# Kernel optimization log

Hardware: AMD Instinct MI355X
Metric: run time of the kernel (lower is better)

The kernel has to match this reference:

```python
import jax, jax.numpy as jnp
import numpy as np


def setup_inputs() -> dict:
    key = jax.random.key(0)
    k1, k2, k3 = jax.random.split(key, 3)
    B, C, H, W, D = 2, 32, 64, 64, 96
    NUM_CLASSES = 2
    features = jax.random.normal(k1, (B, C, H, W, D), dtype=jnp.float32)
    predictions = jax.random.normal(k2, (B, NUM_CLASSES, H, W, D), dtype=jnp.float32)
    targets = jax.random.randint(k3, (B, 1, H, W, D), 0, NUM_CLASSES, dtype=jnp.int64)
    return {"features": features, "predictions": predictions, "targets": targets}


def reference(features, predictions, targets):
    # features: (B,C,H,W,D), predictions: (B,K,H,W,D) logits, targets: (B,1,H,W,D) int
    B, C, H, W, D = features.shape
    K = predictions.shape[1]
    N = H * W * D

    probs = jax.nn.softmax(predictions, axis=1)          # (B,K,H,W,D)
    feat = features.reshape(B, C, N).transpose(0, 2, 1)  # (B,N,C)
    tgt = targets.reshape(B, N)                           # (B,N)
    probs = probs.reshape(B, K, N)                        # (B,K,N)

    onehot = jax.nn.one_hot(tgt, K, dtype=feat.dtype)     # (B,N,K)
    n_pix = onehot.sum(axis=1)                            # (B,K) pixel counts per class
    safe_n = jnp.maximum(n_pix, 1.0)

    # per-class spectral centers: masked mean over pixels
    centers = jnp.einsum('bnk,bnc->bkc', onehot, feat) / safe_n[..., None]  # (B,K,C)

    # gather each pixel's own-class center and confidence
    center_pp = jnp.einsum('bnk,bkc->bnc', onehot, centers)                 # (B,N,C)
    conf = jnp.take_along_axis(probs, tgt[:, None, :], axis=1)[:, 0, :]     # (B,N)

    dist = jnp.linalg.norm(feat - center_pp, axis=-1)     # (B,N) L2 spectral distance
    weighted = dist * conf

    # per-(b,class) mean of weighted distances over that class's pixels
    class_loss = jnp.einsum('bnk,bn->bk', onehot, weighted) / safe_n        # (B,K)

    valid = (n_pix >= 2.0).astype(feat.dtype)             # classes with >=2 pixels
    num_valid = valid.sum()
    total = (class_loss * valid).sum()
    return jnp.where(num_valid > 0, total / jnp.maximum(num_valid, 1.0),
                     jnp.zeros((), dtype=feat.dtype))
```

## Files before the change

### kernel.cpp

```cpp
#include <hip/hip_runtime.h>
#include <math.h>

#define CCH 32
#define KCLS 2
#define BB 2
#define SSEG 32
#define P1_BLOCKS (BB * SSEG * CCH)
#define P2_PER_B 768
#define P2_BLOCKS (BB * P2_PER_B)

#define OFF_PART 0
#define OFF_CNTP (OFF_PART + P1_BLOCKS * 2)
#define OFF_CTR  (OFF_CNTP + BB * SSEG)
#define OFF_CNT  (OFF_CTR + BB * KCLS * CCH)
#define OFF_LOSS (OFF_CNT + BB * KCLS)

__device__ __forceinline__ float waveReduceSum(float v) {
#pragma unroll
    for (int o = 32; o > 0; o >>= 1) v += __shfl_down(v, o);
    return v;
}

__global__ void __launch_bounds__(256) scl_pass1(
    const float* __restrict__ feat, const int* __restrict__ tgt,
    float* __restrict__ part, float* __restrict__ cntPart, int N) {
    const int blk = blockIdx.x;
    const int c = blk & (CCH - 1);
    const int s = (blk >> 5) & (SSEG - 1);
    const int b = blk >> 10;
    const int segVox = N / SSEG;
    const int segQ = segVox / 4;

    const float* fb = feat + ((size_t)(b * CCH + c)) * N + (size_t)s * segVox;
    const int*   tb = tgt + (size_t)b * N + (size_t)s * segVox;

    float s1 = 0.f, st = 0.f, c1 = 0.f;
    for (int q = threadIdx.x; q < segQ; q += 256) {
        const int n = q * 4;
        const int4   t4 = *reinterpret_cast<const int4*>(tb + n);
        const float4 v  = *reinterpret_cast<const float4*>(fb + n);
        const float m1x = t4.x ? 1.f : 0.f;
        const float m1y = t4.y ? 1.f : 0.f;
        const float m1z = t4.z ? 1.f : 0.f;
        const float m1w = t4.w ? 1.f : 0.f;
        st += (v.x + v.y) + (v.z + v.w);
        s1 += v.x * m1x + v.y * m1y + v.z * m1z + v.w * m1w;
        c1 += (m1x + m1y) + (m1z + m1w);
    }

    __shared__ float sm[4][3];
    const int lane = threadIdx.x & 63;
    const int wv   = threadIdx.x >> 6;
    float r1 = waveReduceSum(s1);
    float rt = waveReduceSum(st);
    float rc = waveReduceSum(c1);
    if (lane == 0) { sm[wv][0] = r1; sm[wv][1] = rt; sm[wv][2] = rc; }
    __syncthreads();
    if (threadIdx.x == 0) {
        const float a1 = sm[0][0] + sm[1][0] + sm[2][0] + sm[3][0];
        const float at = sm[0][1] + sm[1][1] + sm[2][1] + sm[3][1];
        part[blk * 2 + 0] = a1;
        part[blk * 2 + 1] = at;
        if (c == 0) {
            const float ac = sm[0][2] + sm[1][2] + sm[2][2] + sm[3][2];
            cntPart[b * SSEG + s] = ac;
        }
    }
}

__global__ void scl_reduce(const float* __restrict__ part,
                           const float* __restrict__ cntPart,
                           float* __restrict__ centers,
                           float* __restrict__ counts, int N) {
    __shared__ float cs[BB * 2];
    const int t = threadIdx.x;
    if (t < BB) {
        float c1 = 0.f;
#pragma unroll
        for (int s = 0; s < SSEG; ++s) c1 += cntPart[t * SSEG + s];
        const float c0 = (float)N - c1;
        cs[t * 2 + 0] = c0; cs[t * 2 + 1] = c1;
        counts[t * 2 + 0] = c0; counts[t * 2 + 1] = c1;
    }
    __syncthreads();
    if (t < BB * CCH) {
        const int b = t >> 5, c = t & 31;
        float s1 = 0.f, stt = 0.f;
#pragma unroll
        for (int s = 0; s < SSEG; ++s) {
            const float* p = part + ((size_t)((b * SSEG + s) * CCH + c)) * 2;
            s1  += p[0];
            stt += p[1];
        }
        const float c0 = cs[b * 2 + 0], c1v = cs[b * 2 + 1];
        centers[(b * KCLS + 0) * CCH + c] = (stt - s1) / fmaxf(c0, 1.f);
        centers[(b * KCLS + 1) * CCH + c] = s1 / fmaxf(c1v, 1.f);
    }
}

__global__ void __launch_bounds__(256) scl_pass2(
    const float* __restrict__ feat, const float* __restrict__ pred,
    const int* __restrict__ tgt, const float* __restrict__ centers,
    float* __restrict__ lossPart, int N) {
    const int blk = blockIdx.x;
    const int b  = (blk >= P2_PER_B) ? 1 : 0;
    const int lb = blk - b * P2_PER_B;

    __shared__ float ctr[KCLS * CCH];
    if (threadIdx.x < KCLS * CCH)
        ctr[threadIdx.x] = centers[b * KCLS * CCH + threadIdx.x];
    __syncthreads();

    const int n = (lb * 256 + threadIdx.x) * 2;
    const float* fb = feat + (size_t)b * CCH * N;
    const float* p0 = pred + (size_t)b * KCLS * N;
    const float* p1 = p0 + N;
    const int*   tb = tgt + (size_t)b * N;

    const int2   t2 = *reinterpret_cast<const int2*>(tb + n);
    const float2 a0 = *reinterpret_cast<const float2*>(p0 + n);
    const float2 a1 = *reinterpret_cast<const float2*>(p1 + n);

    float d2x = 0.f, d2y = 0.f;
#pragma unroll
    for (int c = 0; c < CCH; ++c) {
        const float2 v = *reinterpret_cast<const float2*>(fb + (size_t)c * N + n);
        const float c0 = ctr[c], c1 = ctr[CCH + c];
        float d;
        d = v.x - (t2.x ? c1 : c0); d2x += d * d;
        d = v.y - (t2.y ? c1 : c0); d2y += d * d;
    }

    float l0 = 0.f, l1 = 0.f;
    {
        float mx = fmaxf(a0.x, a1.x);
        float e0 = __expf(a0.x - mx), e1 = __expf(a1.x - mx);
        float cf = (t2.x ? e1 : e0) / (e0 + e1);
        float w  = sqrtf(d2x) * cf;
        l0 += t2.x ? 0.f : w; l1 += t2.x ? w : 0.f;
        mx = fmaxf(a0.y, a1.y);
        e0 = __expf(a0.y - mx); e1 = __expf(a1.y - mx);
        cf = (t2.y ? e1 : e0) / (e0 + e1);
        w  = sqrtf(d2y) * cf;
        l0 += t2.y ? 0.f : w; l1 += t2.y ? w : 0.f;
    }

    __shared__ float sm[4][2];
    const int lane = threadIdx.x & 63;
    const int wv   = threadIdx.x >> 6;
    float r0 = waveReduceSum(l0);
    float r1 = waveReduceSum(l1);
    if (lane == 0) { sm[wv][0] = r0; sm[wv][1] = r1; }
    __syncthreads();
    if (threadIdx.x == 0) {
        lossPart[blk * 2 + 0] = sm[0][0] + sm[1][0] + sm[2][0] + sm[3][0];
        lossPart[blk * 2 + 1] = sm[0][1] + sm[1][1] + sm[2][1] + sm[3][1];
    }
}

__global__ void __launch_bounds__(256) scl_pass3(
    const float* __restrict__ lossPart, const float* __restrict__ counts,
    float* __restrict__ out) {
    float a00 = 0.f, a01 = 0.f, a10 = 0.f, a11 = 0.f;
    for (int blk = threadIdx.x; blk < P2_BLOCKS; blk += 256) {
        const float l0 = lossPart[blk * 2 + 0];
        const float l1 = lossPart[blk * 2 + 1];
        if (blk < P2_PER_B) { a00 += l0; a01 += l1; }
        else                { a10 += l0; a11 += l1; }
    }
    __shared__ float sm[4][4];
    const int lane = threadIdx.x & 63;
    const int wv   = threadIdx.x >> 6;
    float r0 = waveReduceSum(a00);
    float r1 = waveReduceSum(a01);
    float r2 = waveReduceSum(a10);
    float r3 = waveReduceSum(a11);
    if (lane == 0) { sm[wv][0] = r0; sm[wv][1] = r1; sm[wv][2] = r2; sm[wv][3] = r3; }
    __syncthreads();
    if (threadIdx.x == 0) {
        float loss[4];
#pragma unroll
        for (int i = 0; i < 4; ++i)
            loss[i] = sm[0][i] + sm[1][i] + sm[2][i] + sm[3][i];
        float total = 0.f, nv = 0.f;
#pragma unroll
        for (int bk = 0; bk < 4; ++bk) {
            const float cn = counts[bk];
            const float cl = loss[bk] / fmaxf(cn, 1.f);
            if (cn >= 2.f) { total += cl; nv += 1.f; }
        }
        out[0] = (nv > 0.f) ? (total / nv) : 0.f;
    }
}

extern "C" void kernel_launch(void* const* d_in, const int* in_sizes, int n_in,
                              void* d_out, int out_size, void* d_ws, size_t ws_size,
                              hipStream_t stream) {
    const float* feat = (const float*)d_in[0];
    const float* pred = (const float*)d_in[1];
    const int*   tgt  = (const int*)d_in[2];
    float* out = (float*)d_out;

    const int totalVox = in_sizes[2];
    const int N = totalVox / BB;

    float* ws       = (float*)d_ws;
    float* part     = ws + OFF_PART;
    float* cntPart  = ws + OFF_CNTP;
    float* centers  = ws + OFF_CTR;
    float* counts   = ws + OFF_CNT;
    float* lossPart = ws + OFF_LOSS;

    scl_pass1<<<P1_BLOCKS, 256, 0, stream>>>(feat, tgt, part, cntPart, N);
    scl_reduce<<<1, 64, 0, stream>>>(part, cntPart, centers, counts, N);
    scl_pass2<<<P2_BLOCKS, 256, 0, stream>>>(feat, pred, tgt, centers, lossPart, N);
    scl_pass3<<<1, 256, 0, stream>>>(lossPart, counts, out);
}
```

Before: 47.96 us.

## Fold center reduction into pass2 and finalize via last-block ticket

Removes the single-block center-reduction kernel and the final reduction kernel, cutting four launches to two. Each pass2 block now recomputes the per-batch centers from the pass1 partials in shared memory. A global atomic ticket, reset in pass1, lets the last pass2 block do the final loss reduction. This trades two launch gaps and their serialization for redundant small reductions in every pass2 block plus an atomic and threadfence per block.

```diff
diff --git a/kernel.cpp b/kernel.cpp
--- a/kernel.cpp
+++ b/kernel.cpp
@@ -11,9 +11,8 @@
 
 #define OFF_PART 0
 #define OFF_CNTP (OFF_PART + P1_BLOCKS * 2)
-#define OFF_CTR  (OFF_CNTP + BB * SSEG)
-#define OFF_CNT  (OFF_CTR + BB * KCLS * CCH)
-#define OFF_LOSS (OFF_CNT + BB * KCLS)
+#define OFF_LOSS (OFF_CNTP + BB * SSEG)
+#define OFF_TICK (OFF_LOSS + P2_BLOCKS * 2)
 
 __device__ __forceinline__ float waveReduceSum(float v) {
 #pragma unroll
@@ -23,7 +22,10 @@
 
 __global__ void __launch_bounds__(256) scl_pass1(
     const float* __restrict__ feat, const int* __restrict__ tgt,
-    float* __restrict__ part, float* __restrict__ cntPart, int N) {
+    float* __restrict__ part, float* __restrict__ cntPart,
+    unsigned int* __restrict__ ticket, int N) {
+    if (blockIdx.x == 0 && threadIdx.x == 0) *ticket = 0u;
+
     const int blk = blockIdx.x;
     const int c = blk & (CCH - 1);
     const int s = (blk >> 5) & (SSEG - 1);
@@ -57,61 +59,59 @@
     if (lane == 0) { sm[wv][0] = r1; sm[wv][1] = rt; sm[wv][2] = rc; }
     __syncthreads();
     if (threadIdx.x == 0) {
-        const float a1 = sm[0][0] + sm[1][0] + sm[2][0] + sm[3][0];
-        const float at = sm[0][1] + sm[1][1] + sm[2][1] + sm[3][1];
-        part[blk * 2 + 0] = a1;
-        part[blk * 2 + 1] = at;
-        if (c == 0) {
-            const float ac = sm[0][2] + sm[1][2] + sm[2][2] + sm[3][2];
-            cntPart[b * SSEG + s] = ac;
-        }
-    }
-}
-
-__global__ void scl_reduce(const float* __restrict__ part,
-                           const float* __restrict__ cntPart,
-                           float* __restrict__ centers,
-                           float* __restrict__ counts, int N) {
-    __shared__ float cs[BB * 2];
-    const int t = threadIdx.x;
-    if (t < BB) {
-        float c1 = 0.f;
-#pragma unroll
-        for (int s = 0; s < SSEG; ++s) c1 += cntPart[t * SSEG + s];
-        const float c0 = (float)N - c1;
-        cs[t * 2 + 0] = c0; cs[t * 2 + 1] = c1;
-        counts[t * 2 + 0] = c0; counts[t * 2 + 1] = c1;
-    }
-    __syncthreads();
-    if (t < BB * CCH) {
-        const int b = t >> 5, c = t & 31;
-        float s1 = 0.f, stt = 0.f;
-#pragma unroll
-        for (int s = 0; s < SSEG; ++s) {
-            const float* p = part + ((size_t)((b * SSEG + s) * CCH + c)) * 2;
-            s1  += p[0];
-            stt += p[1];
-        }
-        const float c0 = cs[b * 2 + 0], c1v = cs[b * 2 + 1];
-        centers[(b * KCLS + 0) * CCH + c] = (stt - s1) / fmaxf(c0, 1.f);
-        centers[(b * KCLS + 1) * CCH + c] = s1 / fmaxf(c1v, 1.f);
+        part[blk * 2 + 0] = sm[0][0] + sm[1][0] + sm[2][0] + sm[3][0];
+        part[blk * 2 + 1] = sm[0][1] + sm[1][1] + sm[2][1] + sm[3][1];
+        if (c == 0)
+            cntPart[b * SSEG + s] = sm[0][2] + sm[1][2] + sm[2][2] + sm[3][2];
     }
 }
 
 __global__ void __launch_bounds__(256) scl_pass2(
     const float* __restrict__ feat, const float* __restrict__ pred,
-    const int* __restrict__ tgt, const float* __restrict__ centers,
-    float* __restrict__ lossPart, int N) {
+    const int* __restrict__ tgt,
+    const float* __restrict__ part, const float* __restrict__ cntPart,
+    float* __restrict__ lossPart, unsigned int* __restrict__ ticket,
+    float* __restrict__ out, int N) {
     const int blk = blockIdx.x;
     const int b  = (blk >= P2_PER_B) ? 1 : 0;
     const int lb = blk - b * P2_PER_B;
-
+    const int t = threadIdx.x;
+
+    __shared__ float red[64][4];
+    __shared__ float cnt_sm[34];
     __shared__ float ctr[KCLS * CCH];
-    if (threadIdx.x < KCLS * CCH)
-        ctr[threadIdx.x] = centers[b * KCLS * CCH + threadIdx.x];
-    __syncthreads();
-
-    const int n = (lb * 256 + threadIdx.x) * 2;
+    if (t < SSEG) cnt_sm[t] = cntPart[b * SSEG + t];
+    {
+        const int combo = t >> 2;
+        const int quarter = t & 3;
+        const int c = combo >> 1;
+        const int val = combo & 1;
+        const float* p = part + ((size_t)(b * SSEG) * CCH + c) * 2 + val;
+        float s = 0.f;
+#pragma unroll
+        for (int i = 0; i < 8; ++i)
+            s += p[(size_t)(quarter * 8 + i) * CCH * 2];
+        red[combo][quarter] = s;
+    }
+    __syncthreads();
+    if (t == 0) {
+        float c1 = 0.f;
+#pragma unroll
+        for (int i = 0; i < SSEG; ++i) c1 += cnt_sm[i];
+        cnt_sm[32] = c1;
+    }
+    __syncthreads();
+    if (t < CCH) {
+        const float c1 = cnt_sm[32];
+        const float c0 = (float)N - c1;
+        const float s1 = (red[t*2][0] + red[t*2][1]) + (red[t*2][2] + red[t*2][3]);
+        const float st = (red[t*2+1][0] + red[t*2+1][1]) + (red[t*2+1][2] + red[t*2+1][3]);
+        ctr[t]       = (st - s1) / fmaxf(c0, 1.f);
+        ctr[CCH + t] = s1 / fmaxf(c1, 1.f);
+    }
+    __syncthreads();
+
+    const int n = (lb * 256 + t) * 2;
     const float* fb = feat + (size_t)b * CCH * N;
     const float* p0 = pred + (size_t)b * KCLS * N;
     const float* p1 = p0 + N;
@@ -145,49 +145,60 @@
         l0 += t2.y ? 0.f : w; l1 += t2.y ? w : 0.f;
     }
 
-    __shared__ float sm[4][2];
-    const int lane = threadIdx.x & 63;
-    const int wv   = threadIdx.x >> 6;
+    const int lane = t & 63;
+    const int wv   = t >> 6;
     float r0 = waveReduceSum(l0);
     float r1 = waveReduceSum(l1);
-    if (lane == 0) { sm[wv][0] = r0; sm[wv][1] = r1; }
-    __syncthreads();
-    if (threadIdx.x == 0) {
-        lossPart[blk * 2 + 0] = sm[0][0] + sm[1][0] + sm[2][0] + sm[3][0];
-        lossPart[blk * 2 + 1] = sm[0][1] + sm[1][1] + sm[2][1] + sm[3][1];
-    }
-}
-
-__global__ void __launch_bounds__(256) scl_pass3(
-    const float* __restrict__ lossPart, const float* __restrict__ counts,
-    float* __restrict__ out) {
+    __syncthreads();
+    if (lane == 0) { red[wv][0] = r0; red[wv][1] = r1; }
+    __syncthreads();
+
+    __shared__ bool isLast;
+    if (t == 0) {
+        lossPart[blk * 2 + 0] = (red[0][0] + red[1][0]) + (red[2][0] + red[3][0]);
+        lossPart[blk * 2 + 1] = (red[0][1] + red[1][1]) + (red[2][1] + red[3][1]);
+        __threadfence();
+        isLast = (atomicAdd(ticket, 1u) == P2_BLOCKS - 1);
+    }
+    __syncthreads();
+    if (!isLast) return;
+
+    __threadfence();
     float a00 = 0.f, a01 = 0.f, a10 = 0.f, a11 = 0.f;
-    for (int blk = threadIdx.x; blk < P2_BLOCKS; blk += 256) {
-        const float l0 = lossPart[blk * 2 + 0];
-        const float l1 = lossPart[blk * 2 + 1];
-        if (blk < P2_PER_B) { a00 += l0; a01 += l1; }
-        else                { a10 += l0; a11 += l1; }
-    }
-    __shared__ float sm[4][4];
-    const int lane = threadIdx.x & 63;
-    const int wv   = threadIdx.x >> 6;
-    float r0 = waveReduceSum(a00);
-    float r1 = waveReduceSum(a01);
-    float r2 = waveReduceSum(a10);
-    float r3 = waveReduceSum(a11);
-    if (lane == 0) { sm[wv][0] = r0; sm[wv][1] = r1; sm[wv][2] = r2; sm[wv][3] = r3; }
-    __syncthreads();
-    if (threadIdx.x == 0) {
+    for (int i = t; i < P2_BLOCKS; i += 256) {
+        const float l0e = lossPart[i * 2 + 0];
+        const float l1e = lossPart[i * 2 + 1];
+        if (i < P2_PER_B) { a00 += l0e; a01 += l1e; }
+        else              { a10 += l0e; a11 += l1e; }
+    }
+    float q0 = waveReduceSum(a00);
+    float q1 = waveReduceSum(a01);
+    float q2 = waveReduceSum(a10);
+    float q3 = waveReduceSum(a11);
+    __syncthreads();
+    if (lane == 0) { red[wv][0] = q0; red[wv][1] = q1; red[wv][2] = q2; red[wv][3] = q3; }
+    __syncthreads();
+    if (t == 0) {
         float loss[4];
 #pragma unroll
         for (int i = 0; i < 4; ++i)
-            loss[i] = sm[0][i] + sm[1][i] + sm[2][i] + sm[3][i];
+            loss[i] = (red[0][i] + red[1][i]) + (red[2][i] + red[3][i]);
+        float cn[4];
+        {
+            float c1b0 = 0.f, c1b1 = 0.f;
+#pragma unroll
+            for (int i = 0; i < SSEG; ++i) {
+                c1b0 += cntPart[i];
+                c1b1 += cntPart[SSEG + i];
+            }
+            cn[0] = (float)N - c1b0; cn[1] = c1b0;
+            cn[2] = (float)N - c1b1; cn[3] = c1b1;
+        }
         float total = 0.f, nv = 0.f;
 #pragma unroll
         for (int bk = 0; bk < 4; ++bk) {
-            const float cn = counts[bk];
-            const float cl = loss[bk] / fmaxf(cn, 1.f);
-            if (cn >= 2.f) { total += cl; nv += 1.f; }
+            const float cl = loss[bk] / fmaxf(cn[bk], 1.f);
+            if (cn[bk] >= 2.f) { total += cl; nv += 1.f; }
         }
         out[0] = (nv > 0.f) ? (total / nv) : 0.f;
     }
@@ -207,12 +218,10 @@
     float* ws       = (float*)d_ws;
     float* part     = ws + OFF_PART;
     float* cntPart  = ws + OFF_CNTP;
-    float* centers  = ws + OFF_CTR;
-    float* counts   = ws + OFF_CNT;
     float* lossPart = ws + OFF_LOSS;
-
-    scl_pass1<<<P1_BLOCKS, 256, 0, stream>>>(feat, tgt, part, cntPart, N);
-    scl_reduce<<<1, 64, 0, stream>>>(part, cntPart, centers, counts, N);
-    scl_pass2<<<P2_BLOCKS, 256, 0, stream>>>(feat, pred, tgt, centers, lossPart, N);
-    scl_pass3<<<1, 256, 0, stream>>>(lossPart, counts, out);
-}
+    unsigned int* ticket = (unsigned int*)(ws + OFF_TICK);
+
+    scl_pass1<<<P1_BLOCKS, 256, 0, stream>>>(feat, tgt, part, cntPart, ticket, N);
+    scl_pass2<<<P2_BLOCKS, 256, 0, stream>>>(feat, pred, tgt, part, cntPart,
+                                             lossPart, ticket, out, N);
+}
```

Measured after the change: 92.86 us. 93.6% more time.
